# Optimization experiments

Measured on AMD Instinct MI355X. Metric: run time of the kernel, lower is better.

The kernel has to match this reference:

```python
import jax, jax.numpy as jnp
import numpy as np

N = 50000
E = 600000
IN = 128
H = 4
F = 32  # per-head out; concat output = H*F = 128
NEG_SLOPE = 0.2


def setup_inputs() -> dict:
    key = jax.random.key(0)
    k1, k2, k3, k4, k5, k6 = jax.random.split(key, 6)
    x = jax.random.normal(k1, (N, IN), dtype=jnp.float32)
    edge_index = jax.random.randint(k2, (2, E), 0, N, dtype=jnp.int64)
    W = jax.random.normal(k3, (IN, H * F), dtype=jnp.float32) * 0.05
    att_src = jax.random.normal(k4, (H, F), dtype=jnp.float32) * 0.05
    att_dst = jax.random.normal(k5, (H, F), dtype=jnp.float32) * 0.05
    bias = jnp.zeros((H * F,), dtype=jnp.float32)
    return {"x": x, "edge_index": edge_index, "W": W,
            "att_src": att_src, "att_dst": att_dst, "bias": bias}


def reference(x, edge_index, W, att_src, att_dst, bias):
    n = x.shape[0]
    # add self loops (PyG GATConv default)
    loop = jnp.arange(n, dtype=edge_index.dtype)
    src = jnp.concatenate([edge_index[0], loop])
    dst = jnp.concatenate([edge_index[1], loop])

    h = (x @ W).reshape(n, H, F)                      # [N,H,F]
    a_s = jnp.einsum('nhf,hf->nh', h, att_src)        # [N,H]
    a_d = jnp.einsum('nhf,hf->nh', h, att_dst)        # [N,H]

    e = a_s[src] + a_d[dst]                           # [E',H]
    e = jax.nn.leaky_relu(e, NEG_SLOPE)
    # segment softmax over incoming edges of each destination node
    m = jax.ops.segment_max(e, dst, num_segments=n)   # [N,H]
    m = jnp.where(jnp.isfinite(m), m, 0.0)
    ex = jnp.exp(e - m[dst])                          # [E',H]
    denom = jax.ops.segment_sum(ex, dst, num_segments=n)  # [N,H]
    alpha = ex / denom[dst]                           # [E',H]

    msgs = alpha[:, :, None] * h[src]                 # [E',H,F]
    out = jax.ops.segment_sum(msgs, dst, num_segments=n)  # [N,H,F]
    out = out.reshape(n, H * F) + bias
    return jax.nn.relu(out)
```

## Files before the change

### kernel.cpp

```cpp
#include <hip/hip_runtime.h>

#define NEG_SLOPE 0.2f
#define CAP 64
#define NB 256
#define MAXB 4096
#define A_EDGES 2048
#define A_BLOCKS 293
#define GEMM_BLOCKS 391

typedef __attribute__((ext_vector_type(8))) short short8;
typedef __attribute__((ext_vector_type(4))) float f32x4;

__device__ __forceinline__ unsigned short f2bf(float f) {
    union { float f; unsigned int i; } v; v.f = f;
    unsigned int r = v.i + 0x7FFF + ((v.i >> 16) & 1);
    return (unsigned short)(r >> 16);
}
__device__ __forceinline__ float lrelu(float v) {
    return v > 0.f ? v : NEG_SLOPE * v;
}

__global__ void gat_prep(const float* __restrict__ W,
                         const float* __restrict__ att_src,
                         const float* __restrict__ att_dst,
                         unsigned short* __restrict__ wt,
                         int* __restrict__ bcur)
{
    int i = blockIdx.x * blockDim.x + threadIdx.x;
    if (i < NB) bcur[i] = 0;
    if (i >= 144 * 128) return;
    int r = i >> 7, k = i & 127;
    float v = 0.f;
    if (r < 128) {
        v = W[k * 128 + r];
    } else if (r < 136) {
        int hh = (r - 128) & 3;
        const float* att = (r < 132) ? att_src : att_dst;
        float s = 0.f;
        #pragma unroll 8
        for (int f = 0; f < 32; f++)
            s = fmaf(W[k * 128 + hh * 32 + f], att[hh * 32 + f], s);
        v = s;
    }
    wt[i] = f2bf(v);
}

__global__ __launch_bounds__(256) void gat_mega(
    const float* __restrict__ x, const unsigned short* __restrict__ wt,
    const int* __restrict__ ei, unsigned short* __restrict__ hb,
    float* __restrict__ a_s, float* __restrict__ a_d,
    int* __restrict__ bcur, unsigned int* __restrict__ bbuf, int nE, int n)
{
    const int bid = blockIdx.x;
    if (bid < A_BLOCKS) {
        __shared__ int hist[NB];
        __shared__ int gbase[NB];
        const int tid = threadIdx.x;
        hist[tid] = 0;
        __syncthreads();

        int base = bid * A_EDGES + tid * 8;
        int sreg[8], dreg[8], rreg[8];
        bool act = (base + 8 <= nE);
        if (act) {
            int4 s0 = ((const int4*)(ei + base))[0];
            int4 s1 = ((const int4*)(ei + base))[1];
            int4 d0 = ((const int4*)(ei + nE + base))[0];
            int4 d1 = ((const int4*)(ei + nE + base))[1];
            sreg[0]=s0.x; sreg[1]=s0.y; sreg[2]=s0.z; sreg[3]=s0.w;
            sreg[4]=s1.x; sreg[5]=s1.y; sreg[6]=s1.z; sreg[7]=s1.w;
            dreg[0]=d0.x; dreg[1]=d0.y; dreg[2]=d0.z; dreg[3]=d0.w;
            dreg[4]=d1.x; dreg[5]=d1.y; dreg[6]=d1.z; dreg[7]=d1.w;
            #pragma unroll
            for (int j = 0; j < 8; j++)
                rreg[j] = atomicAdd(&hist[dreg[j] >> 8], 1);
        }
        __syncthreads();
        {
            int h = hist[tid];
            gbase[tid] = (h > 0) ? atomicAdd(&bcur[tid], h) : 0;
        }
        __syncthreads();
        if (act) {
            #pragma unroll
            for (int j = 0; j < 8; j++) {
                int b = dreg[j] >> 8;
                int idx = gbase[b] + rreg[j];
                if (idx < MAXB)
                    bbuf[(size_t)b * MAXB + idx] =
                        ((unsigned int)dreg[j] << 16) | (unsigned int)sreg[j];
            }
        }
        return;
    }
    const int wave = threadIdx.x >> 6, lane = threadIdx.x & 63;
    const int quad = lane >> 4, l15 = lane & 15;
    const int m0 = (bid - A_BLOCKS) * 128 + wave * 32;
    if (m0 >= n) return;
    const int row0 = m0 + l15;
    const int row1 = min(m0 + 16 + l15, n - 1);

    f32x4 acc0[9], acc1[9];
    #pragma unroll
    for (int t = 0; t < 9; t++) {
        acc0[t] = (f32x4){0.f, 0.f, 0.f, 0.f};
        acc1[t] = (f32x4){0.f, 0.f, 0.f, 0.f};
    }

    const float* xr0 = x + (size_t)row0 * 128 + quad * 8;
    const float* xr1 = x + (size_t)row1 * 128 + quad * 8;
    #pragma unroll
    for (int kk = 0; kk < 4; ++kk) {
        float4 f0 = ((const float4*)(xr0 + kk * 32))[0];
        float4 f1 = ((const float4*)(xr0 + kk * 32))[1];
        float4 g0 = ((const float4*)(xr1 + kk * 32))[0];
        float4 g1 = ((const float4*)(xr1 + kk * 32))[1];
        short8 afrag0, afrag1;
        afrag0[0] = (short)f2bf(f0.x); afrag0[1] = (short)f2bf(f0.y);
        afrag0[2] = (short)f2bf(f0.z); afrag0[3] = (short)f2bf(f0.w);
        afrag0[4] = (short)f2bf(f1.x); afrag0[5] = (short)f2bf(f1.y);
        afrag0[6] = (short)f2bf(f1.z); afrag0[7] = (short)f2bf(f1.w);
        afrag1[0] = (short)f2bf(g0.x); afrag1[1] = (short)f2bf(g0.y);
        afrag1[2] = (short)f2bf(g0.z); afrag1[3] = (short)f2bf(g0.w);
        afrag1[4] = (short)f2bf(g1.x); afrag1[5] = (short)f2bf(g1.y);
        afrag1[6] = (short)f2bf(g1.z); afrag1[7] = (short)f2bf(g1.w);
        #pragma unroll
        for (int t = 0; t < 9; ++t) {
            short8 bfrag = *(const short8*)(wt + (size_t)(t * 16 + l15) * 128 + kk * 32 + quad * 8);
            acc0[t] = __builtin_amdgcn_mfma_f32_16x16x32_bf16(afrag0, bfrag, acc0[t], 0, 0, 0);
            acc1[t] = __builtin_amdgcn_mfma_f32_16x16x32_bf16(afrag1, bfrag, acc1[t], 0, 0, 0);
        }
    }

    #pragma unroll
    for (int t = 0; t < 8; ++t)
        #pragma unroll
        for (int r = 0; r < 4; ++r) {
            int orow0 = m0 + quad * 4 + r;
            hb[(size_t)orow0 * 128 + t * 16 + l15] = f2bf(acc0[t][r]);
            int orow1 = orow0 + 16;
            if (orow1 < n)
                hb[(size_t)orow1 * 128 + t * 16 + l15] = f2bf(acc1[t][r]);
        }
    if (l15 < 8) {
        float* dst = (l15 < 4) ? a_s : a_d;
        int hh = l15 & 3;
        #pragma unroll
        for (int r = 0; r < 4; ++r) {
            int orow0 = m0 + quad * 4 + r;
            dst[(size_t)orow0 * 4 + hh] = acc0[8][r];
            int orow1 = orow0 + 16;
            if (orow1 < n)
                dst[(size_t)orow1 * 4 + hh] = acc1[8][r];
        }
    }
}

__global__ __launch_bounds__(1024) void gat_ell_build(
    const int* __restrict__ bcur, const unsigned int* __restrict__ bbuf,
    unsigned short* __restrict__ csr, int* __restrict__ cnt, int n)
{
    __shared__ int lcnt[NB];
    const int b = blockIdx.x, tid = threadIdx.x;
    if (tid < NB) lcnt[tid] = 0;
    __syncthreads();
    int count = min(bcur[b], MAXB);
    int i = tid * 4;
    if (i < count) {
        uint4 u4 = ((const uint4*)(bbuf + (size_t)b * MAXB))[tid];
        unsigned int uu[4] = {u4.x, u4.y, u4.z, u4.w};
        #pragma unroll
        for (int j = 0; j < 4; j++) {
            if (i + j < count) {
                unsigned int u = uu[j];
                int d = (int)(u >> 16);
                int slot = atomicAdd(&lcnt[d & 255], 1);
                if (slot < CAP)
                    csr[(size_t)d * CAP + slot] = (unsigned short)(u & 0xFFFFu);
            }
        }
    }
    __syncthreads();
    if (tid < NB) {
        int d = (b << 8) + tid;
        if (d < n) cnt[d] = lcnt[tid];
    }
}

__global__ __launch_bounds__(256) void gat_accumulate(
    const int* __restrict__ cnt, const unsigned short* __restrict__ csr,
    const float4* __restrict__ a_s4, const float4* __restrict__ a_d4,
    const uint4* __restrict__ h4, const float* __restrict__ bias,
    float* __restrict__ out, int n)
{
    __shared__ float wtab[4][256];
    __shared__ int   stab[4][64];
    int lane = threadIdx.x & 63;
    int wslot = threadIdx.x >> 6;
    int d = blockIdx.x * 4 + wslot;
    if (d >= n) return;

    int deg  = min(cnt[d], CAP - 1);
    int degi = deg + 1;
    int slotv = (lane < deg) ? (int)csr[(size_t)d * CAP + lane] : d;
    stab[wslot][lane] = slotv;

    float4 ad = a_d4[d];
    float4 w4 = {0.f, 0.f, 0.f, 0.f};
    if (lane < degi) {
        float4 as = a_s4[slotv];
        w4.x = __expf(lrelu(as.x + ad.x));
        w4.y = __expf(lrelu(as.y + ad.y));
        w4.z = __expf(lrelu(as.z + ad.z));
        w4.w = __expf(lrelu(as.w + ad.w));
    }
    ((float4*)wtab[wslot])[lane] = w4;

    int quad = lane >> 4, c = lane & 15;
    int head = c >> 2;
    const float* wrow = wtab[wslot];
    const int*   srow = stab[wslot];

    float acc[8] = {0.f,0.f,0.f,0.f,0.f,0.f,0.f,0.f};
    float den = 0.f;

    for (int j = 0; j < degi; j += 16) {
        int je[4]; int sv[4]; uint4 hv[4];
        #pragma unroll
        for (int u = 0; u < 4; u++) {
            je[u] = j + 4 * u + quad;
            sv[u] = srow[je[u]];
        }
        #pragma unroll
        for (int u = 0; u < 4; u++)
            if (je[u] < degi)
                hv[u] = h4[(size_t)sv[u] * 16 + c];
        #pragma unroll
        for (int u = 0; u < 4; u++) {
            if (je[u] < degi) {
                float w = wrow[je[u] * 4 + head];
                union { unsigned int i; float f; } lo, hi;
                #pragma unroll
                for (int k = 0; k < 4; k++) {
                    unsigned int uu = (&hv[u].x)[k];
                    lo.i = uu << 16; hi.i = uu & 0xFFFF0000u;
                    acc[2*k]   = fmaf(w, lo.f, acc[2*k]);
                    acc[2*k+1] = fmaf(w, hi.f, acc[2*k+1]);
                }
                den += w;
            }
        }
    }

    #pragma unroll
    for (int m = 16; m <= 32; m <<= 1) {
        #pragma unroll
        for (int k = 0; k < 8; k++) acc[k] += __shfl_xor(acc[k], m);
        den += __shfl_xor(den, m);
    }

    if (quad == 0) {
        float inv = 1.f / den;
        float4 b0 = ((const float4*)bias)[2*c];
        float4 b1 = ((const float4*)bias)[2*c + 1];
        float4 o0, o1;
        o0.x = fmaxf(acc[0]*inv + b0.x, 0.f); o0.y = fmaxf(acc[1]*inv + b0.y, 0.f);
        o0.z = fmaxf(acc[2]*inv + b0.z, 0.f); o0.w = fmaxf(acc[3]*inv + b0.w, 0.f);
        o1.x = fmaxf(acc[4]*inv + b1.x, 0.f); o1.y = fmaxf(acc[5]*inv + b1.y, 0.f);
        o1.z = fmaxf(acc[6]*inv + b1.z, 0.f); o1.w = fmaxf(acc[7]*inv + b1.w, 0.f);
        ((float4*)out)[(size_t)d * 32 + 2*c]     = o0;
        ((float4*)out)[(size_t)d * 32 + 2*c + 1] = o1;
    }
}

extern "C" void kernel_launch(void* const* d_in, const int* in_sizes, int n_in,
                              void* d_out, int out_size, void* d_ws, size_t ws_size,
                              hipStream_t stream)
{
    const float* x       = (const float*)d_in[0];
    const int*   ei      = (const int*)d_in[1];
    const float* W       = (const float*)d_in[2];
    const float* att_src = (const float*)d_in[3];
    const float* att_dst = (const float*)d_in[4];
    const float* bias    = (const float*)d_in[5];

    const int n  = in_sizes[0] / 128;
    const int nE = in_sizes[1] / 2;

    char* wsb = (char*)d_ws;
    unsigned short* hb  = (unsigned short*)wsb;
    unsigned short* wt  = hb + (size_t)n * 128;
    float* a_s = (float*)(wt + 144 * 128);
    float* a_d = a_s + (size_t)n * 4;
    int*   cnt  = (int*)(a_d + (size_t)n * 4);
    int*   bcur = cnt + n;
    unsigned short* csr = (unsigned short*)(bcur + NB);
    unsigned int*  bbuf = (unsigned int*)(csr + (size_t)n * CAP);
    float* out = (float*)d_out;

    const int nbkt = (n + 255) >> 8;

    gat_prep<<<(144 * 128 + 255) / 256, 256, 0, stream>>>(W, att_src, att_dst,
                                                          wt, bcur);
    gat_mega<<<A_BLOCKS + GEMM_BLOCKS, 256, 0, stream>>>(x, wt, ei, hb, a_s,
                                                         a_d, bcur, bbuf, nE, n);
    gat_ell_build<<<nbkt, 1024, 0, stream>>>(bcur, bbuf, csr, cnt, n);
    gat_accumulate<<<(n + 3) / 4, 256, 0, stream>>>(cnt, csr, (const float4*)a_s,
                                                    (const float4*)a_d,
                                                    (const uint4*)hb, bias, out, n);
}
```

Baseline: 144.2 us.

## Build ELL adjacency directly with global atomics, dropping bucket pass

Replaces the two-stage bucketed graph build (a shared-memory histogram into per-bucket buffers, then a separate ELL build kernel) with direct global atomicAdd on each destination's count, writing the source index straight into the ELL slot. This removes one kernel launch, the intermediate bucket buffer traffic and the block-level syncs. In exchange it issues one global atomic per edge to random addresses, which may contend and serialize. gat_prep now zeroes per-node counts, which needs a larger grid.

Result: slower. 160.2 us (+11.0%).

```diff
diff --git a/kernel.cpp b/kernel.cpp
--- a/kernel.cpp
+++ b/kernel.cpp
@@ -2,8 +2,6 @@
 
 #define NEG_SLOPE 0.2f
 #define CAP 64
-#define NB 256
-#define MAXB 4096
 #define A_EDGES 2048
 #define A_BLOCKS 293
 #define GEMM_BLOCKS 391
@@ -24,10 +22,10 @@
                          const float* __restrict__ att_src,
                          const float* __restrict__ att_dst,
                          unsigned short* __restrict__ wt,
-                         int* __restrict__ bcur)
+                         int* __restrict__ cnt, int n)
 {
     int i = blockIdx.x * blockDim.x + threadIdx.x;
-    if (i < NB) bcur[i] = 0;
+    if (i < n) cnt[i] = 0;
     if (i >= 144 * 128) return;
     int r = i >> 7, k = i & 127;
     float v = 0.f;
@@ -49,47 +47,28 @@
     const float* __restrict__ x, const unsigned short* __restrict__ wt,
     const int* __restrict__ ei, unsigned short* __restrict__ hb,
     float* __restrict__ a_s, float* __restrict__ a_d,
-    int* __restrict__ bcur, unsigned int* __restrict__ bbuf, int nE, int n)
+    int* __restrict__ cnt, unsigned short* __restrict__ csr, int nE, int n)
 {
     const int bid = blockIdx.x;
     if (bid < A_BLOCKS) {
-        __shared__ int hist[NB];
-        __shared__ int gbase[NB];
         const int tid = threadIdx.x;
-        hist[tid] = 0;
-        __syncthreads();
-
         int base = bid * A_EDGES + tid * 8;
-        int sreg[8], dreg[8], rreg[8];
-        bool act = (base + 8 <= nE);
-        if (act) {
+        if (base + 8 <= nE) {
             int4 s0 = ((const int4*)(ei + base))[0];
             int4 s1 = ((const int4*)(ei + base))[1];
             int4 d0 = ((const int4*)(ei + nE + base))[0];
             int4 d1 = ((const int4*)(ei + nE + base))[1];
-            sreg[0]=s0.x; sreg[1]=s0.y; sreg[2]=s0.z; sreg[3]=s0.w;
-            sreg[4]=s1.x; sreg[5]=s1.y; sreg[6]=s1.z; sreg[7]=s1.w;
-            dreg[0]=d0.x; dreg[1]=d0.y; dreg[2]=d0.z; dreg[3]=d0.w;
-            dreg[4]=d1.x; dreg[5]=d1.y; dreg[6]=d1.z; dreg[7]=d1.w;
+            int sreg[8] = {s0.x, s0.y, s0.z, s0.w, s1.x, s1.y, s1.z, s1.w};
+            int dreg[8] = {d0.x, d0.y, d0.z, d0.w, d1.x, d1.y, d1.z, d1.w};
+            int slot[8];
             #pragma unroll
             for (int j = 0; j < 8; j++)
-                rreg[j] = atomicAdd(&hist[dreg[j] >> 8], 1);
-        }
-        __syncthreads();
-        {
-            int h = hist[tid];
-            gbase[tid] = (h > 0) ? atomicAdd(&bcur[tid], h) : 0;
-        }
-        __syncthreads();
-        if (act) {
+                slot[j] = atomicAdd(&cnt[dreg[j]], 1);
             #pragma unroll
-            for (int j = 0; j < 8; j++) {
-                int b = dreg[j] >> 8;
-                int idx = gbase[b] + rreg[j];
-                if (idx < MAXB)
-                    bbuf[(size_t)b * MAXB + idx] =
-                        ((unsigned int)dreg[j] << 16) | (unsigned int)sreg[j];
-            }
+            for (int j = 0; j < 8; j++)
+                if (slot[j] < CAP)
+                    csr[(size_t)dreg[j] * CAP + slot[j]] =
+                        (unsigned short)sreg[j];
         }
         return;
     }
@@ -156,37 +135,6 @@
     }
 }
 
-__global__ __launch_bounds__(1024) void gat_ell_build(
-    const int* __restrict__ bcur, const unsigned int* __restrict__ bbuf,
-    unsigned short* __restrict__ csr, int* __restrict__ cnt, int n)
-{
-    __shared__ int lcnt[NB];
-    const int b = blockIdx.x, tid = threadIdx.x;
-    if (tid < NB) lcnt[tid] = 0;
-    __syncthreads();
-    int count = min(bcur[b], MAXB);
-    int i = tid * 4;
-    if (i < count) {
-        uint4 u4 = ((const uint4*)(bbuf + (size_t)b * MAXB))[tid];
-        unsigned int uu[4] = {u4.x, u4.y, u4.z, u4.w};
-        #pragma unroll
-        for (int j = 0; j < 4; j++) {
-            if (i + j < count) {
-                unsigned int u = uu[j];
-                int d = (int)(u >> 16);
-                int slot = atomicAdd(&lcnt[d & 255], 1);
-                if (slot < CAP)
-                    csr[(size_t)d * CAP + slot] = (unsigned short)(u & 0xFFFFu);
-            }
-        }
-    }
-    __syncthreads();
-    if (tid < NB) {
-        int d = (b << 8) + tid;
-        if (d < n) cnt[d] = lcnt[tid];
-    }
-}
-
 __global__ __launch_bounds__(256) void gat_accumulate(
     const int* __restrict__ cnt, const unsigned short* __restrict__ csr,
     const float4* __restrict__ a_s4, const float4* __restrict__ a_d4,
@@ -293,18 +241,13 @@
     float* a_s = (float*)(wt + 144 * 128);
     float* a_d = a_s + (size_t)n * 4;
     int*   cnt  = (int*)(a_d + (size_t)n * 4);
-    int*   bcur = cnt + n;
-    unsigned short* csr = (unsigned short*)(bcur + NB);
-    unsigned int*  bbuf = (unsigned int*)(csr + (size_t)n * CAP);
+    unsigned short* csr = (unsigned short*)(cnt + n);
     float* out = (float*)d_out;
 
-    const int nbkt = (n + 255) >> 8;
-
-    gat_prep<<<(144 * 128 + 255) / 256, 256, 0, stream>>>(W, att_src, att_dst,
-                                                          wt, bcur);
+    gat_prep<<<(n + 255) / 256, 256, 0, stream>>>(W, att_src, att_dst,
+                                                  wt, cnt, n);
     gat_mega<<<A_BLOCKS + GEMM_BLOCKS, 256, 0, stream>>>(x, wt, ei, hb, a_s,
-                                                         a_d, bcur, bbuf, nE, n);
-    gat_ell_build<<<nbkt, 1024, 0, stream>>>(bcur, bbuf, csr, cnt, n);
+                                                         a_d, cnt, csr, nE, n);
     gat_accumulate<<<(n + 3) / 4, 256, 0, stream>>>(cnt, csr, (const float4*)a_s,
                                                     (const float4*)a_d,
                                                     (const uint4*)hb, bias, out, n);
```
